# Kernel tuning notes

Hardware: AMD Instinct MI355X
Metric: run time of the kernel (lower is better)

Reference implementation:

```python
import math
import jax, jax.numpy as jnp
import numpy as np

LM_DAMPING = 1e-3
MOTION_LAMBDA = 1.0
LM_ITERS = (2, 3, 4)


def _skew(w):  # (B,3) -> (B,3,3)
    z = jnp.zeros_like(w[:, 0])
    return jnp.stack([z, -w[:, 2], w[:, 1],
                      w[:, 2], z, -w[:, 0],
                      -w[:, 1], w[:, 0], z], axis=-1).reshape(-1, 3, 3)


def _se3_exp(xi):  # (B,6) -> (B,4,4)
    t, w = xi[:, :3], xi[:, 3:]
    theta = jnp.clip(jnp.linalg.norm(w, axis=-1, keepdims=True), 1e-8, None)  # (B,1)
    K = _skew(w / theta)
    eye = jnp.eye(3, dtype=xi.dtype)
    st = jnp.sin(theta)[:, :, None]          # (B,1,1)
    ct = (1.0 - jnp.cos(theta))[:, :, None]
    KK = K @ K
    R = eye + st * K + ct * KK
    th = jnp.clip(theta[:, :, None], 1e-8, None)
    V = eye + (ct / th) * K + (1.0 - st / th) * KK
    t_out = (V @ t[..., None])[..., 0]
    B = xi.shape[0]
    T = jnp.tile(jnp.eye(4, dtype=xi.dtype)[None], (B, 1, 1))
    T = T.at[:, :3, :3].set(R).at[:, :3, 3].set(t_out)
    return T


def _se3_log(T):  # (B,4,4) -> (B,6)
    R, t = T[:, :3, :3], T[:, :3, 3]
    cos_a = (R[:, 0, 0] + R[:, 1, 1] + R[:, 2, 2] - 1.0) / 2.0
    theta = jnp.arccos(jnp.clip(cos_a, -1.0 + 1e-7, 1.0 - 1e-7))
    small = jnp.abs(theta) < 1e-6
    th = jnp.clip(theta, 1e-8, None)
    w = jnp.stack([R[:, 2, 1] - R[:, 1, 2],
                   R[:, 0, 2] - R[:, 2, 0],
                   R[:, 1, 0] - R[:, 0, 1]], axis=-1)
    w = w / (2.0 * jnp.clip(jnp.sin(th), 1e-8, None))[:, None] * th[:, None]
    w = jnp.where(small[:, None], 0.0, w)
    return jnp.concatenate([t, w], axis=-1)


def _sample_one(feat, gx, gy):
    # feat (C,H,W); gx,gy (P,) normalized in [-1,1]; align_corners=False, border padding
    C, H, W = feat.shape
    x = jnp.clip(((gx + 1.0) * W - 1.0) / 2.0, 0.0, W - 1)
    y = jnp.clip(((gy + 1.0) * H - 1.0) / 2.0, 0.0, H - 1)
    x0 = jnp.floor(x); y0 = jnp.floor(y)
    x1 = jnp.minimum(x0 + 1.0, W - 1); y1 = jnp.minimum(y0 + 1.0, H - 1)
    wx = x - x0; wy = y - y0
    x0i, x1i = x0.astype(jnp.int32), x1.astype(jnp.int32)
    y0i, y1i = y0.astype(jnp.int32), y1.astype(jnp.int32)
    f00 = feat[:, y0i, x0i]; f01 = feat[:, y0i, x1i]
    f10 = feat[:, y1i, x0i]; f11 = feat[:, y1i, x1i]
    return (f00 * (1 - wx) * (1 - wy) + f01 * wx * (1 - wy)
            + f10 * (1 - wx) * wy + f11 * wx * wy)  # (C,P)

_sample = jax.vmap(_sample_one, in_axes=(0, 0, 0))


def _generate_hypotheses(T_pred, key):
    rng = jnp.arange(-11.0, 13.0, 2.0, dtype=jnp.float32)  # 12 values
    pg, yg = jnp.meshgrid(rng, rng, indexing='ij')
    pitch = pg.reshape(-1) * (math.pi / 180.0)
    yaw = yg.reshape(-1) * (math.pi / 180.0)
    M = pitch.shape[0]  # 144
    t_noise = jax.random.normal(key, (M, 3), dtype=jnp.float32) * 1.0  # translation_std
    xi = jnp.stack([t_noise[:, 0], t_noise[:, 1], t_noise[:, 2],
                    jnp.zeros(M, jnp.float32), pitch, yaw], axis=-1)
    dT = _se3_exp(xi)  # (M,4,4)
    return jnp.einsum('mij,bjk->bmik', dT, T_pred)  # (B,M,4,4)


def _residuals(T, q_feat, r_feat, q_unc, geo, K, level):
    # T (B,M,4,4); fallback path evaluates only first min(M,16) hypotheses
    B, M = T.shape[:2]
    _, C, H, W = q_feat.shape
    scale = 1.0 / (4.0 / 2 ** level)
    Ks = jnp.concatenate([K[:, :2] * scale, K[:, 2:]], axis=1)
    M16 = min(M, 16)
    Tm = T[:, :M16]  # (B,16,4,4)
    N = geo.shape[1]
    pts_h = jnp.concatenate([geo, jnp.ones((B, N, 1), geo.dtype)], axis=-1)  # (B,N,4)
    pts_cam = jnp.einsum('bmij,bnj->bmni', Tm[:, :, :3, :], pts_h)  # (B,16,N,3)
    z = jnp.clip(pts_cam[..., 2:3], 1e-6, None)
    xy = pts_cam[..., :2] / z
    fx = Ks[:, 0, 0][:, None, None]; fy = Ks[:, 1, 1][:, None, None]
    cx = Ks[:, 0, 2][:, None, None]; cy = Ks[:, 1, 2][:, None, None]
    u = fx * xy[..., 0] + cx
    v = fy * xy[..., 1] + cy
    gx = (2.0 * u / max(W - 1, 1) - 1.0).reshape(B, M16 * N)
    gy = (2.0 * v / max(H - 1, 1) - 1.0).reshape(B, M16 * N)
    qs = _sample(q_feat, gx, gy).reshape(B, C, M16, N)
    rs = _sample(r_feat, gx, gy).reshape(B, C, M16, N)
    diff2 = (qs - rs) ** 2
    unc = _sample(q_unc, gx, gy).reshape(B, 1, M16, N)
    res = (diff2 * unc).sum(axis=1).mean(axis=-1)  # (B,16)
    return jnp.zeros((B, M), T.dtype).at[:, :M16].set(res)


def reference(T_pred, geo_anchors, intrinsics, q0, q1, q2, r0, r1, r2, u0, u1, u2):
    key = jax.random.key(42)
    B = T_pred.shape[0]
    T_cur = _generate_hypotheses(T_pred, jax.random.fold_in(key, 0))
    M = T_cur.shape[1]
    q_feats = (q0, q1, q2); r_feats = (r0, r1, r2); uncs = (u0, u1, u2)
    costs = jnp.zeros((B, M), T_pred.dtype)
    for level, n_iters in enumerate(LM_ITERS):
        for it in range(n_iters):
            res = _residuals(T_cur, q_feats[level], r_feats[level], uncs[level],
                             geo_anchors, intrinsics, level)
            damping = LM_DAMPING * 0.5 ** level
            noise = jax.random.normal(jax.random.fold_in(key, 100 + level * 10 + it),
                                      (B, M, 6), dtype=T_pred.dtype)
            step = -damping * res[..., None] * noise * 0.01
            delta = _se3_exp(step.reshape(B * M, 6)).reshape(B, M, 4, 4)
            T_cur = delta @ T_cur
            costs = res
    # motion-constrained selection: C_total = C_photo + lambda * ||log(T_ref T_pred^-1)||
    T_rel = T_cur @ jnp.linalg.inv(T_pred)[:, None]
    geod = jnp.linalg.norm(_se3_log(T_rel.reshape(B * M, 4, 4)), axis=-1).reshape(B, M)
    total = costs + MOTION_LAMBDA * geod
    idx = jnp.argmin(total, axis=1)
    T_best = jnp.take_along_axis(T_cur, idx[:, None, None, None], axis=1)[:, 0]
    return T_best, costs


def setup_inputs() -> dict:
    key = jax.random.key(0)
    ks = jax.random.split(key, 16)
    B, N = 8, 500
    # valid SE(3) predicted poses (small perturbation of identity)
    T_pred = _se3_exp(jax.random.normal(ks[0], (B, 6), jnp.float32) * 0.1)
    # 3D anchors in front of the camera (z ~ 6)
    geo = jax.random.uniform(ks[1], (B, N, 3), jnp.float32, -2.0, 2.0)
    geo = geo.at[..., 2].add(6.0)
    K = jnp.tile(jnp.array([[200.0, 0.0, 128.0],
                            [0.0, 200.0, 96.0],
                            [0.0, 0.0, 1.0]], jnp.float32)[None], (B, 1, 1))
    shapes_f = [(B, 128, 48, 64), (B, 64, 96, 128), (B, 32, 192, 256)]
    q = [jax.random.normal(ks[2 + i], s, jnp.float32) for i, s in enumerate(shapes_f)]
    r = [jax.random.normal(ks[5 + i], s, jnp.float32) for i, s in enumerate(shapes_f)]
    u = [jax.random.uniform(ks[8 + i], (s[0], 1, s[2], s[3]), jnp.float32)
         for i, s in enumerate(shapes_f)]
    return {"T_pred": T_pred, "geo_anchors": geo, "intrinsics": K,
            "q0": q[0], "q1": q[1], "q2": q[2],
            "r0": r[0], "r1": r[1], "r2": r[2],
            "u0": u[0], "u1": u[1], "u2": u[2]}
```

## Files before the change

### kernel.cpp

```cpp
#include <hip/hip_runtime.h>
#include <stdint.h>
#include <math.h>

#define JAX_PARTITIONABLE 1

#define NB 8
#define NM 144
#define NM16 16
#define NPTS 500
#define GP 16

__host__ __device__ __forceinline__ uint32_t rotl32(uint32_t x, int r) {
    return (x << r) | (x >> (32 - r));
}

__host__ __device__ inline void threefry2x32(uint32_t k0, uint32_t k1,
                                             uint32_t x0, uint32_t x1,
                                             uint32_t& o0, uint32_t& o1) {
    uint32_t ks2 = k0 ^ k1 ^ 0x1BD11BDAu;
    x0 += k0; x1 += k1;
    const int RA[4] = {13, 15, 26, 6};
    const int RB[4] = {17, 29, 16, 24};
#define R4(ROT) { x0 += x1; x1 = rotl32(x1, ROT[0]); x1 ^= x0; \
                  x0 += x1; x1 = rotl32(x1, ROT[1]); x1 ^= x0; \
                  x0 += x1; x1 = rotl32(x1, ROT[2]); x1 ^= x0; \
                  x0 += x1; x1 = rotl32(x1, ROT[3]); x1 ^= x0; }
    R4(RA); x0 += k1;  x1 += ks2 + 1u;
    R4(RB); x0 += ks2; x1 += k0 + 2u;
    R4(RA); x0 += k0;  x1 += k1 + 3u;
    R4(RB); x0 += k1;  x1 += ks2 + 4u;
    R4(RA); x0 += ks2; x1 += k0 + 5u;
#undef R4
    o0 = x0; o1 = x1;
}

__device__ __forceinline__ float erfinv32(float x) {
    float w = -log1pf(-x * x);
    float p;
    if (w < 5.0f) {
        w = w - 2.5f;
        p = 2.81022636e-08f;
        p = fmaf(p, w, 3.43273939e-07f);
        p = fmaf(p, w, -3.5233877e-06f);
        p = fmaf(p, w, -4.39150654e-06f);
        p = fmaf(p, w, 0.00021858087f);
        p = fmaf(p, w, -0.00125372503f);
        p = fmaf(p, w, -0.00417768164f);
        p = fmaf(p, w, 0.246640727f);
        p = fmaf(p, w, 1.50140941f);
    } else {
        w = sqrtf(w) - 3.0f;
        p = -0.000200214257f;
        p = fmaf(p, w, 0.000100950558f);
        p = fmaf(p, w, 0.00134934322f);
        p = fmaf(p, w, -0.00367342844f);
        p = fmaf(p, w, 0.00573950773f);
        p = fmaf(p, w, -0.0076224613f);
        p = fmaf(p, w, 0.00943887047f);
        p = fmaf(p, w, 1.00167406f);
        p = fmaf(p, w, 2.83297682f);
    }
    return p * x;
}

__device__ __forceinline__ float jax_normal(uint32_t k0, uint32_t k1,
                                            uint32_t idx, uint32_t half) {
    uint32_t o0, o1, bits;
#if JAX_PARTITIONABLE
    threefry2x32(k0, k1, 0u, idx, o0, o1);
    bits = o0 ^ o1;
#else
    if (idx < half) { threefry2x32(k0, k1, idx, idx + half, o0, o1); bits = o0; }
    else            { threefry2x32(k0, k1, idx - half, idx, o0, o1); bits = o1; }
#endif
    uint32_t fb = (bits >> 9) | 0x3F800000u;
    float f = __uint_as_float(fb) - 1.0f;
    const float lo = -0.99999994f;
    float u = f * (1.0f - lo) + lo;
    u = fmaxf(lo, u);
    return 1.4142135623730951f * erfinv32(u);
}

__device__ inline void se3_exp6(const float xi[6], float T[12]) {
    float tx = xi[0], ty = xi[1], tz = xi[2];
    float wx = xi[3], wy = xi[4], wz = xi[5];
    float nrm = sqrtf(wx * wx + wy * wy + wz * wz);
    float theta = fmaxf(nrm, 1e-8f);
    float kx = wx / theta, ky = wy / theta, kz = wz / theta;
    float K[9] = {0.0f, -kz, ky, kz, 0.0f, -kx, -ky, kx, 0.0f};
    float st = sinf(theta);
    float ct = 1.0f - cosf(theta);
    float KK[9];
    for (int i = 0; i < 3; i++)
        for (int j = 0; j < 3; j++)
            KK[i * 3 + j] = K[i * 3 + 0] * K[0 + j] + K[i * 3 + 1] * K[3 + j] + K[i * 3 + 2] * K[6 + j];
    float a = ct / theta;
    float bb = 1.0f - st / theta;
    float R[9], V[9];
    for (int i = 0; i < 3; i++)
        for (int j = 0; j < 3; j++) {
            float e = (i == j) ? 1.0f : 0.0f;
            R[i * 3 + j] = e + st * K[i * 3 + j] + ct * KK[i * 3 + j];
            V[i * 3 + j] = e + a * K[i * 3 + j] + bb * KK[i * 3 + j];
        }
    float t0 = V[0] * tx + V[1] * ty + V[2] * tz;
    float t1 = V[3] * tx + V[4] * ty + V[5] * tz;
    float t2 = V[6] * tx + V[7] * ty + V[8] * tz;
    T[0] = R[0]; T[1] = R[1]; T[2] = R[2];  T[3] = t0;
    T[4] = R[3]; T[5] = R[4]; T[6] = R[5];  T[7] = t1;
    T[8] = R[6]; T[9] = R[7]; T[10] = R[8]; T[11] = t2;
}

__device__ inline void compose44(const float dT[12], const float P[16], float Tn[16]) {
    for (int i = 0; i < 3; i++)
        for (int j = 0; j < 4; j++)
            Tn[i * 4 + j] = dT[i * 4 + 0] * P[0 + j] + dT[i * 4 + 1] * P[4 + j] +
                            dT[i * 4 + 2] * P[8 + j] + dT[i * 4 + 3] * P[12 + j];
    Tn[12] = 0.0f; Tn[13] = 0.0f; Tn[14] = 0.0f; Tn[15] = 1.0f;
}

__device__ inline void make_hypothesis(int m, const float* P, uint32_t hk0, uint32_t hk1,
                                       float Tn[16]) {
    float tn[3];
    for (int c = 0; c < 3; c++)
        tn[c] = jax_normal(hk0, hk1, (uint32_t)(m * 3 + c), 216u);
    int gi = m / 12, gj = m % 12;
    const float d2r = (float)(M_PI / 180.0);
    float xi[6] = {tn[0], tn[1], tn[2], 0.0f,
                   (float)(2 * gi - 11) * d2r, (float)(2 * gj - 11) * d2r};
    float dT[12];
    se3_exp6(xi, dT);
    compose44(dT, P, Tn);
}

__device__ inline void se3_exp6d(const double xi[6], double T[12]) {
    double tx = xi[0], ty = xi[1], tz = xi[2];
    double wx = xi[3], wy = xi[4], wz = xi[5];
    double nrm = sqrt(wx * wx + wy * wy + wz * wz);
    double theta = fmax(nrm, 1e-8);
    double kx = wx / theta, ky = wy / theta, kz = wz / theta;
    double K[9] = {0.0, -kz, ky, kz, 0.0, -kx, -ky, kx, 0.0};
    double st = sin(theta);
    double ct = 1.0 - cos(theta);
    double KK[9];
    for (int i = 0; i < 3; i++)
        for (int j = 0; j < 3; j++)
            KK[i * 3 + j] = K[i * 3 + 0] * K[0 + j] + K[i * 3 + 1] * K[3 + j] + K[i * 3 + 2] * K[6 + j];
    double a = ct / theta;
    double bb = 1.0 - st / theta;
    double R[9], V[9];
    for (int i = 0; i < 3; i++)
        for (int j = 0; j < 3; j++) {
            double e = (i == j) ? 1.0 : 0.0;
            R[i * 3 + j] = e + st * K[i * 3 + j] + ct * KK[i * 3 + j];
            V[i * 3 + j] = e + a * K[i * 3 + j] + bb * KK[i * 3 + j];
        }
    double t0 = V[0] * tx + V[1] * ty + V[2] * tz;
    double t1 = V[3] * tx + V[4] * ty + V[5] * tz;
    double t2 = V[6] * tx + V[7] * ty + V[8] * tz;
    T[0] = R[0]; T[1] = R[1]; T[2] = R[2];  T[3] = t0;
    T[4] = R[3]; T[5] = R[4]; T[6] = R[5];  T[7] = t1;
    T[8] = R[6]; T[9] = R[7]; T[10] = R[8]; T[11] = t2;
}

__device__ inline void compose44d(const double dT[12], const double P[16], double Tn[16]) {
    for (int i = 0; i < 3; i++)
        for (int j = 0; j < 4; j++)
            Tn[i * 4 + j] = dT[i * 4 + 0] * P[0 + j] + dT[i * 4 + 1] * P[4 + j] +
                            dT[i * 4 + 2] * P[8 + j] + dT[i * 4 + 3] * P[12 + j];
    Tn[12] = 0.0; Tn[13] = 0.0; Tn[14] = 0.0; Tn[15] = 1.0;
}

__device__ inline void make_hypothesis_d(int m, const double* P, uint32_t hk0, uint32_t hk1,
                                         double Tn[16]) {
    float tn[3];
    for (int c = 0; c < 3; c++)
        tn[c] = jax_normal(hk0, hk1, (uint32_t)(m * 3 + c), 216u);
    int gi = m / 12, gj = m % 12;
    const float d2r = (float)(M_PI / 180.0);
    float pf = (float)(2 * gi - 11) * d2r;
    float yf = (float)(2 * gj - 11) * d2r;
    double xi[6] = {(double)tn[0], (double)tn[1], (double)tn[2], 0.0,
                    (double)pf, (double)yf};
    double dT[12];
    se3_exp6d(xi, dT);
    compose44d(dT, P, Tn);
}

struct IterKeys { uint32_t k0[9]; uint32_t k1[9]; float damping[9]; };

template <int C, int H, int W, int PX, int GRP>
__device__ void gram_body(const float* __restrict__ q, const float* __restrict__ r,
                          const float* __restrict__ u, float* __restrict__ G,
                          float* part, int blk) {
    constexpr int HW = H * W;
    constexpr int TPB = HW / PX;
    constexpr int CPG = C / GRP;
    const int b = blk / TPB;
    const int tile = blk % TPB;
    const int tid = threadIdx.x;
    const int g = tid / PX;
    const int p = tid % PX;
    const int px = tile * PX + p;
    const int y = px / W, x = px % W;
    const int x1 = (x + 1 < W) ? x + 1 : W - 1;
    const int y1 = (y + 1 < H) ? y + 1 : H - 1;
    const int i00 = y * W + x,  i01 = y * W + x1;
    const int i10 = y1 * W + x, i11 = y1 * W + x1;

    const size_t cb = ((size_t)b * C + g * CPG) * HW;
    const float* qp = q + cb;
    const float* rp = r + cb;
    float acc[10];
#pragma unroll
    for (int i = 0; i < 10; i++) acc[i] = 0.0f;
#pragma unroll 4
    for (int c = 0; c < CPG; c++) {
        float d00 = qp[i00] - rp[i00];
        float d01 = qp[i01] - rp[i01];
        float d10 = qp[i10] - rp[i10];
        float d11 = qp[i11] - rp[i11];
        acc[0] = fmaf(d00, d00, acc[0]);
        acc[1] = fmaf(d00, d01, acc[1]);
        acc[2] = fmaf(d00, d10, acc[2]);
        acc[3] = fmaf(d00, d11, acc[3]);
        acc[4] = fmaf(d01, d01, acc[4]);
        acc[5] = fmaf(d01, d10, acc[5]);
        acc[6] = fmaf(d01, d11, acc[6]);
        acc[7] = fmaf(d10, d10, acc[7]);
        acc[8] = fmaf(d10, d11, acc[8]);
        acc[9] = fmaf(d11, d11, acc[9]);
        qp += HW; rp += HW;
    }
    if (GRP > 1) {
#pragma unroll
        for (int i = 0; i < 10; i++) part[(g * 10 + i) * PX + p] = acc[i];
        __syncthreads();
        if (tid < PX) {
#pragma unroll
            for (int i = 0; i < 10; i++) {
                float s = part[i * PX + p];
                for (int gg = 1; gg < GRP; gg++) s += part[(gg * 10 + i) * PX + p];
                acc[i] = s;
            }
        }
    }
    if (tid < PX) {
        const size_t ub = (size_t)b * HW;
        float u00 = u[ub + i00], u01 = u[ub + i01];
        float u10 = u[ub + i10], u11 = u[ub + i11];
        size_t base = ((size_t)b * HW + px) * GP;
        float4 g0 = {acc[0], acc[1], acc[2], acc[3]};
        float4 g1 = {acc[4], acc[5], acc[6], acc[7]};
        float4 g2 = {acc[8], acc[9], u00, u01};
        float4 g3 = {u10, u11, 0.0f, 0.0f};
        *(float4*)(G + base + 0)  = g0;
        *(float4*)(G + base + 4)  = g1;
        *(float4*)(G + base + 8)  = g2;
        *(float4*)(G + base + 12) = g3;
    }
}

#define NBLK0 384
#define NBLK1 768
#define NBLK2 1536

__global__ __launch_bounds__(256) void gram_fused_kernel(
    const float* __restrict__ q0, const float* __restrict__ r0, const float* __restrict__ u0,
    float* __restrict__ G0,
    const float* __restrict__ q1, const float* __restrict__ r1, const float* __restrict__ u1,
    float* __restrict__ G1,
    const float* __restrict__ q2, const float* __restrict__ r2, const float* __restrict__ u2,
    float* __restrict__ G2) {
    __shared__ float part[2560];
    const int blk = blockIdx.x;
    if (blk < NBLK0)
        gram_body<128, 48, 64, 64, 4>(q0, r0, u0, G0, part, blk);
    else if (blk < NBLK0 + NBLK1)
        gram_body<64, 96, 128, 128, 2>(q1, r1, u1, G1, part, blk - NBLK0);
    else
        gram_body<32, 192, 256, 256, 1>(q2, r2, u2, G2, part, blk - NBLK0 - NBLK1);
}

template <int H, int W>
__device__ void run_level_gram(const float* __restrict__ Gb,
                               float fx, float fy, float cx, float cy,
                               const float* geoS, float* Tsh, float* red, float* resS,
                               float* stepS, float* out, int b, int m,
                               const IterKeys& iks, int firstIter, int niter) {
    const int tid = threadIdx.x;
    for (int it = 0; it < niter; it++) {
        const int iter = firstIter + it;
        float acc = 0.0f;
        if (tid < NPTS) {
            float px = geoS[tid * 3], py = geoS[tid * 3 + 1], pz = geoS[tid * 3 + 2];
            float X = Tsh[0] * px + Tsh[1] * py + Tsh[2]  * pz + Tsh[3];
            float Y = Tsh[4] * px + Tsh[5] * py + Tsh[6]  * pz + Tsh[7];
            float Z = Tsh[8] * px + Tsh[9] * py + Tsh[10] * pz + Tsh[11];
            float z = fmaxf(Z, 1e-6f);
            float uu = fx * (X / z) + cx;
            float vv = fy * (Y / z) + cy;
            float gx = 2.0f * uu / (float)(W - 1) - 1.0f;
            float gy = 2.0f * vv / (float)(H - 1) - 1.0f;
            float x = fminf(fmaxf(((gx + 1.0f) * (float)W - 1.0f) * 0.5f, 0.0f), (float)(W - 1));
            float y = fminf(fmaxf(((gy + 1.0f) * (float)H - 1.0f) * 0.5f, 0.0f), (float)(H - 1));
            float x0f = floorf(x), y0f = floorf(y);
            float wx = x - x0f, wy = y - y0f;
            int x0i = (int)x0f, y0i = (int)y0f;
            int i00 = y0i * W + x0i;
            float w00 = (1.0f - wx) * (1.0f - wy), w01 = wx * (1.0f - wy);
            float w10 = (1.0f - wx) * wy,          w11 = wx * wy;
            const float* Gp = Gb + (size_t)i00 * GP;
            float4 g0 = *(const float4*)(Gp + 0);
            float4 g1 = *(const float4*)(Gp + 4);
            float4 g2 = *(const float4*)(Gp + 8);
            float4 g3 = *(const float4*)(Gp + 12);
            float uval = w00 * g2.z + w01 * g2.w + w10 * g3.x + w11 * g3.y;
            float val = w00 * w00 * g0.x + w01 * w01 * g1.x +
                        w10 * w10 * g1.w + w11 * w11 * g2.y +
                        2.0f * (w00 * w01 * g0.y + w00 * w10 * g0.z + w00 * w11 * g0.w +
                                w01 * w10 * g1.y + w01 * w11 * g1.z + w10 * w11 * g2.x);
            acc = uval * val;
        }
        float v = acc;
        for (int off = 32; off > 0; off >>= 1) v += __shfl_down(v, off, 64);
        if ((tid & 63) == 0) red[tid >> 6] = v;
        __syncthreads();
        if (tid == 0) {
            float s = 0.0f;
            for (int w = 0; w < 8; w++) s += red[w];
            float res = s / 500.0f;
            *resS = res;
            if (iter == 8) out[128 + b * NM + m] = res;
        }
        __syncthreads();
        if (tid < 6) {
            uint32_t fi = (uint32_t)((b * NM + m) * 6 + tid);
            float nz = jax_normal(iks.k0[iter], iks.k1[iter], fi, 3456u);
            stepS[tid] = (((-iks.damping[iter]) * (*resS)) * nz) * 0.01f;
        }
        __syncthreads();
        if (tid == 0) {
            float xi[6];
            for (int j = 0; j < 6; j++) xi[j] = stepS[j];
            float dT[12];
            se3_exp6(xi, dT);
            float Told[16];
            for (int k = 0; k < 16; k++) Told[k] = Tsh[k];
            float Tn[16];
            compose44(dT, Told, Tn);
            for (int k = 0; k < 16; k++) Tsh[k] = Tn[k];
        }
        __syncthreads();
    }
}

__global__ __launch_bounds__(512) void evolve_kernel_gram(
    const float* __restrict__ T_pred, const float* __restrict__ geo,
    const float* __restrict__ Kmat,
    const float* __restrict__ G0, const float* __restrict__ G1, const float* __restrict__ G2,
    float* __restrict__ Tws, float* __restrict__ out,
    uint32_t hk0, uint32_t hk1, IterKeys iks) {
    const int bm = blockIdx.x;
    const int b = bm & 7;
    const int m = bm >> 3;
    const int tid = threadIdx.x;

    __shared__ float Tsh[16];
    __shared__ float geoS[NPTS * 3];
    __shared__ float red[8];
    __shared__ float resS;
    __shared__ float stepS[6];

    for (int i = tid; i < NPTS * 3; i += 512) geoS[i] = geo[b * NPTS * 3 + i];

    if (tid == 0) {
        float P[16];
        for (int k = 0; k < 16; k++) P[k] = T_pred[b * 16 + k];
        float Tn[16];
        make_hypothesis(m, P, hk0, hk1, Tn);
        for (int k = 0; k < 16; k++) Tsh[k] = Tn[k];
    }
    __syncthreads();

    float K00 = Kmat[b * 9 + 0], K02 = Kmat[b * 9 + 2];
    float K11 = Kmat[b * 9 + 4], K12 = Kmat[b * 9 + 5];

    run_level_gram<48, 64>(G0 + (size_t)b * 48 * 64 * GP,
                           K00 * 0.25f, K11 * 0.25f, K02 * 0.25f, K12 * 0.25f,
                           geoS, Tsh, red, &resS, stepS, out, b, m, iks, 0, 2);
    run_level_gram<96, 128>(G1 + (size_t)b * 96 * 128 * GP,
                            K00 * 0.5f, K11 * 0.5f, K02 * 0.5f, K12 * 0.5f,
                            geoS, Tsh, red, &resS, stepS, out, b, m, iks, 2, 3);
    run_level_gram<192, 256>(G2 + (size_t)b * 192 * 256 * GP,
                             K00, K11, K02, K12,
                             geoS, Tsh, red, &resS, stepS, out, b, m, iks, 5, 4);

    if (tid < 16) Tws[(size_t)(b * NM16 + m) * 16 + tid] = Tsh[tid];
}

template <int C, int H, int W>
__device__ void run_level_nchw(const float* __restrict__ qb, const float* __restrict__ rb,
                               const float* __restrict__ ub,
                               float fx, float fy, float cx, float cy,
                               const float* geoS, float* Tsh, float* red, float* resS,
                               float* stepS, float* out, int b, int m,
                               const IterKeys& iks, int firstIter, int niter) {
    const int tid = threadIdx.x;
    const int HW = H * W;
    for (int it = 0; it < niter; it++) {
        const int iter = firstIter + it;
        float acc = 0.0f;
        if (tid < NPTS) {
            float px = geoS[tid * 3], py = geoS[tid * 3 + 1], pz = geoS[tid * 3 + 2];
            float X = Tsh[0] * px + Tsh[1] * py + Tsh[2]  * pz + Tsh[3];
            float Y = Tsh[4] * px + Tsh[5] * py + Tsh[6]  * pz + Tsh[7];
            float Z = Tsh[8] * px + Tsh[9] * py + Tsh[10] * pz + Tsh[11];
            float z = fmaxf(Z, 1e-6f);
            float uu = fx * (X / z) + cx;
            float vv = fy * (Y / z) + cy;
            float gx = 2.0f * uu / (float)(W - 1) - 1.0f;
            float gy = 2.0f * vv / (float)(H - 1) - 1.0f;
            float x = fminf(fmaxf(((gx + 1.0f) * (float)W - 1.0f) * 0.5f, 0.0f), (float)(W - 1));
            float y = fminf(fmaxf(((gy + 1.0f) * (float)H - 1.0f) * 0.5f, 0.0f), (float)(H - 1));
            float x0f = floorf(x), y0f = floorf(y);
            float x1f = fminf(x0f + 1.0f, (float)(W - 1));
            float y1f = fminf(y0f + 1.0f, (float)(H - 1));
            float wx = x - x0f, wy = y - y0f;
            int x0i = (int)x0f, x1i = (int)x1f, y0i = (int)y0f, y1i = (int)y1f;
            int i00 = y0i * W + x0i, i01 = y0i * W + x1i;
            int i10 = y1i * W + x0i, i11 = y1i * W + x1i;
            float w00 = (1.0f - wx) * (1.0f - wy), w01 = wx * (1.0f - wy);
            float w10 = (1.0f - wx) * wy,          w11 = wx * wy;
            float uval = ub[i00] * w00 + ub[i01] * w01 + ub[i10] * w10 + ub[i11] * w11;
            const float* qp = qb;
            const float* rp = rb;
#pragma unroll 4
            for (int c = 0; c < C; c++) {
                float qv = qp[i00] * w00 + qp[i01] * w01 + qp[i10] * w10 + qp[i11] * w11;
                float rv = rp[i00] * w00 + rp[i01] * w01 + rp[i10] * w10 + rp[i11] * w11;
                float d = qv - rv;
                acc += uval * (d * d);
                qp += HW; rp += HW;
            }
        }
        float v = acc;
        for (int off = 32; off > 0; off >>= 1) v += __shfl_down(v, off, 64);
        if ((tid & 63) == 0) red[tid >> 6] = v;
        __syncthreads();
        if (tid == 0) {
            float s = 0.0f;
            for (int w = 0; w < 8; w++) s += red[w];
            float res = s / 500.0f;
            *resS = res;
            if (iter == 8) out[128 + b * NM + m] = res;
        }
        __syncthreads();
        if (tid < 6) {
            uint32_t fi = (uint32_t)((b * NM + m) * 6 + tid);
            float nz = jax_normal(iks.k0[iter], iks.k1[iter], fi, 3456u);
            stepS[tid] = (((-iks.damping[iter]) * (*resS)) * nz) * 0.01f;
        }
        __syncthreads();
        if (tid == 0) {
            float xi[6];
            for (int j = 0; j < 6; j++) xi[j] = stepS[j];
            float dT[12];
            se3_exp6(xi, dT);
            float Told[16];
            for (int k = 0; k < 16; k++) Told[k] = Tsh[k];
            float Tn[16];
            compose44(dT, Told, Tn);
            for (int k = 0; k < 16; k++) Tsh[k] = Tn[k];
        }
        __syncthreads();
    }
}

__global__ __launch_bounds__(512) void evolve_kernel_nchw(
    const float* __restrict__ T_pred, const float* __restrict__ geo,
    const float* __restrict__ Kmat,
    const float* __restrict__ q0, const float* __restrict__ q1, const float* __restrict__ q2,
    const float* __restrict__ r0, const float* __restrict__ r1, const float* __restrict__ r2,
    const float* __restrict__ u0, const float* __restrict__ u1, const float* __restrict__ u2,
    float* __restrict__ Tws, float* __restrict__ out,
    uint32_t hk0, uint32_t hk1, IterKeys iks) {
    const int bm = blockIdx.x;
    const int b = bm >> 4;
    const int m = bm & 15;
    const int tid = threadIdx.x;

    __shared__ float Tsh[16];
    __shared__ float geoS[NPTS * 3];
    __shared__ float red[8];
    __shared__ float resS;
    __shared__ float stepS[6];

    for (int i = tid; i < NPTS * 3; i += 512) geoS[i] = geo[b * NPTS * 3 + i];

    if (tid == 0) {
        float P[16];
        for (int k = 0; k < 16; k++) P[k] = T_pred[b * 16 + k];
        float Tn[16];
        make_hypothesis(m, P, hk0, hk1, Tn);
        for (int k = 0; k < 16; k++) Tsh[k] = Tn[k];
    }
    __syncthreads();

    float K00 = Kmat[b * 9 + 0], K02 = Kmat[b * 9 + 2];
    float K11 = Kmat[b * 9 + 4], K12 = Kmat[b * 9 + 5];

    run_level_nchw<128, 48, 64>(q0 + (size_t)b * 128 * 48 * 64, r0 + (size_t)b * 128 * 48 * 64,
                                u0 + (size_t)b * 48 * 64,
                                K00 * 0.25f, K11 * 0.25f, K02 * 0.25f, K12 * 0.25f,
                                geoS, Tsh, red, &resS, stepS, out, b, m, iks, 0, 2);
    run_level_nchw<64, 96, 128>(q1 + (size_t)b * 64 * 96 * 128, r1 + (size_t)b * 64 * 96 * 128,
                                u1 + (size_t)b * 96 * 128,
                                K00 * 0.5f, K11 * 0.5f, K02 * 0.5f, K12 * 0.5f,
                                geoS, Tsh, red, &resS, stepS, out, b, m, iks, 2, 3);
    run_level_nchw<32, 192, 256>(q2 + (size_t)b * 32 * 192 * 256, r2 + (size_t)b * 32 * 192 * 256,
                                 u2 + (size_t)b * 192 * 256,
                                 K00, K11, K02, K12,
                                 geoS, Tsh, red, &resS, stepS, out, b, m, iks, 5, 4);

    if (tid < 16) Tws[(size_t)bm * 16 + tid] = Tsh[tid];
}

__global__ __launch_bounds__(192) void finalize_kernel(
    const float* __restrict__ T_pred, const float* __restrict__ Tws,
    float* __restrict__ out, uint32_t hk0, uint32_t hk1) {
    const int b = blockIdx.x;
    const int tid = threadIdx.x;
    __shared__ double Pm[16];
    __shared__ double inv[12];
    __shared__ double totals[NM];
    __shared__ int bestm_sh;

    if (tid < 16) Pm[tid] = (double)T_pred[b * 16 + tid];
    __syncthreads();
    if (tid == 0) {
        for (int k = 0; k < 3; k++)
            for (int j = 0; j < 3; j++) inv[k * 4 + j] = Pm[j * 4 + k];
        for (int k = 0; k < 3; k++)
            inv[k * 4 + 3] = -(Pm[0 * 4 + k] * Pm[3] + Pm[1 * 4 + k] * Pm[7] + Pm[2 * 4 + k] * Pm[11]);
    }
    __syncthreads();

    double Tc[16];
    if (tid < NM) {
        double cost;
        if (tid < NM16) {
            for (int k = 0; k < 16; k++) Tc[k] = (double)Tws[(size_t)(b * NM16 + tid) * 16 + k];
            cost = (double)out[128 + b * NM + tid];
        } else {
            make_hypothesis_d(tid, Pm, hk0, hk1, Tc);
            cost = 0.0;
            out[128 + b * NM + tid] = 0.0f;
        }
        double Tr[12];
        for (int i = 0; i < 3; i++)
            for (int j = 0; j < 4; j++)
                Tr[i * 4 + j] = Tc[i * 4 + 0] * inv[0 + j] + Tc[i * 4 + 1] * inv[4 + j] +
                                Tc[i * 4 + 2] * inv[8 + j] + ((j == 3) ? Tc[i * 4 + 3] : 0.0);
        double cos_a = (Tr[0] + Tr[5] + Tr[10] - 1.0) * 0.5;
        cos_a = fmin(fmax(cos_a, -1.0 + 1e-7), 1.0 - 1e-7);
        double theta = acos(cos_a);
        double th = fmax(theta, 1e-8);
        double s2 = 2.0 * fmax(sin(th), 1e-8);
        double w0 = (Tr[2 * 4 + 1] - Tr[1 * 4 + 2]) / s2 * th;
        double w1 = (Tr[0 * 4 + 2] - Tr[2 * 4 + 0]) / s2 * th;
        double w2 = (Tr[1 * 4 + 0] - Tr[0 * 4 + 1]) / s2 * th;
        double t0 = Tr[3], t1 = Tr[7], t2 = Tr[11];
        double geod = sqrt(t0 * t0 + t1 * t1 + t2 * t2 + w0 * w0 + w1 * w1 + w2 * w2);
        totals[tid] = cost + geod;
    }
    __syncthreads();
    if (tid == 0) {
        int best = 0;
        double bv = totals[0];
        for (int mm = 1; mm < NM; mm++) {
            if (totals[mm] < bv) { bv = totals[mm]; best = mm; }
        }
        bestm_sh = best;
    }
    __syncthreads();
    if (tid == bestm_sh) {
        for (int k = 0; k < 16; k++) out[b * 16 + k] = (float)Tc[k];
    }
}

extern "C" void kernel_launch(void* const* d_in, const int* in_sizes, int n_in,
                              void* d_out, int out_size, void* d_ws, size_t ws_size,
                              hipStream_t stream) {
    (void)in_sizes; (void)n_in; (void)out_size;
    const float* T_pred = (const float*)d_in[0];
    const float* geo    = (const float*)d_in[1];
    const float* K      = (const float*)d_in[2];
    const float* q0 = (const float*)d_in[3];
    const float* q1 = (const float*)d_in[4];
    const float* q2 = (const float*)d_in[5];
    const float* r0 = (const float*)d_in[6];
    const float* r1 = (const float*)d_in[7];
    const float* r2 = (const float*)d_in[8];
    const float* u0 = (const float*)d_in[9];
    const float* u1 = (const float*)d_in[10];
    const float* u2 = (const float*)d_in[11];
    float* out = (float*)d_out;

    float* Tws = (float*)d_ws;
    const size_t nG0 = (size_t)NB * 48 * 64 * GP;
    const size_t nG1 = (size_t)NB * 96 * 128 * GP;
    const size_t nG2 = (size_t)NB * 192 * 256 * GP;
    float* G0 = Tws + 2048;
    float* G1 = G0 + nG0;
    float* G2 = G1 + nG1;
    const size_t need = (2048 + nG0 + nG1 + nG2) * sizeof(float);

    uint32_t hk0, hk1;
    threefry2x32(0u, 42u, 0u, 0u, hk0, hk1);
    IterKeys iks;
    const int seeds[9] = {100, 101, 110, 111, 112, 120, 121, 122, 123};
    const float damp[9] = {0.001f, 0.001f, 0.0005f, 0.0005f, 0.0005f,
                           0.00025f, 0.00025f, 0.00025f, 0.00025f};
    for (int i = 0; i < 9; i++) {
        threefry2x32(0u, 42u, 0u, (uint32_t)seeds[i], iks.k0[i], iks.k1[i]);
        iks.damping[i] = damp[i];
    }

    if (ws_size >= need) {
        gram_fused_kernel<<<dim3(NBLK0 + NBLK1 + NBLK2), dim3(256), 0, stream>>>(
            q0, r0, u0, G0, q1, r1, u1, G1, q2, r2, u2, G2);
        evolve_kernel_gram<<<dim3(NB * NM16), dim3(512), 0, stream>>>(
            T_pred, geo, K, G0, G1, G2, Tws, out, hk0, hk1, iks);
    } else {
        evolve_kernel_nchw<<<dim3(NB * NM16), dim3(512), 0, stream>>>(
            T_pred, geo, K, q0, q1, q2, r0, r1, r2, u0, u1, u2, Tws, out, hk0, hk1, iks);
    }
    finalize_kernel<<<dim3(NB), dim3(192), 0, stream>>>(T_pred, Tws, out, hk0, hk1);
}
```

Before: 274.3 us.

## Vectorize gram precompute: four pixels per thread with float4 loads and lane shuffles

Each thread in the gram precompute now handles four adjacent pixels. It loads q, r and u rows with float4 and gets the right-neighbour value from the next lane via __shfl_down instead of issuing separate scalar loads for the x+1 neighbour. This cuts redundant global loads and the block count by four, but uses 40 accumulators per thread and more shared memory for the cross-group reduction, which may lower occupancy. Correctness at wave boundaries relies on four-pixel groups never crossing a row end except at the edge flag, which holds because each row width is a multiple of 4 times 64.

```diff
diff --git a/kernel.cpp b/kernel.cpp
--- a/kernel.cpp
+++ b/kernel.cpp
@@ -189,81 +189,117 @@
 
 struct IterKeys { uint32_t k0[9]; uint32_t k1[9]; float damping[9]; };
 
-template <int C, int H, int W, int PX, int GRP>
-__device__ void gram_body(const float* __restrict__ q, const float* __restrict__ r,
-                          const float* __restrict__ u, float* __restrict__ G,
-                          float* part, int blk) {
+template <int C, int H, int W, int GRP>
+__device__ void gram_body_v(const float* __restrict__ q, const float* __restrict__ r,
+                            const float* __restrict__ u, float* __restrict__ G,
+                            float* part, int blk) {
     constexpr int HW = H * W;
-    constexpr int TPB = HW / PX;
+    constexpr int PT = 256 / GRP;
+    constexpr int PPB = PT * 4;
+    constexpr int TPB = HW / PPB;
     constexpr int CPG = C / GRP;
     const int b = blk / TPB;
     const int tile = blk % TPB;
     const int tid = threadIdx.x;
-    const int g = tid / PX;
-    const int p = tid % PX;
-    const int px = tile * PX + p;
-    const int y = px / W, x = px % W;
-    const int x1 = (x + 1 < W) ? x + 1 : W - 1;
+    const int g = tid / PT;
+    const int p = tid % PT;
+    const int px0 = tile * PPB + p * 4;
+    const int y = px0 / W;
+    const int x0 = px0 - y * W;
     const int y1 = (y + 1 < H) ? y + 1 : H - 1;
-    const int i00 = y * W + x,  i01 = y * W + x1;
-    const int i10 = y1 * W + x, i11 = y1 * W + x1;
-
-    const size_t cb = ((size_t)b * C + g * CPG) * HW;
-    const float* qp = q + cb;
-    const float* rp = r + cb;
-    float acc[10];
-#pragma unroll
-    for (int i = 0; i < 10; i++) acc[i] = 0.0f;
-#pragma unroll 4
+    const bool edge = (x0 + 4 >= W);
+
+    const int rb0 = y * W + x0;
+    const int rb1 = y1 * W + x0;
+    const float* qp = q + ((size_t)b * C + (size_t)g * CPG) * HW;
+    const float* rp = r + ((size_t)b * C + (size_t)g * CPG) * HW;
+
+    float acc[4][10];
+#pragma unroll
+    for (int j = 0; j < 4; j++)
+#pragma unroll
+        for (int i = 0; i < 10; i++) acc[j][i] = 0.0f;
+
+#pragma unroll 2
     for (int c = 0; c < CPG; c++) {
-        float d00 = qp[i00] - rp[i00];
-        float d01 = qp[i01] - rp[i01];
-        float d10 = qp[i10] - rp[i10];
-        float d11 = qp[i11] - rp[i11];
-        acc[0] = fmaf(d00, d00, acc[0]);
-        acc[1] = fmaf(d00, d01, acc[1]);
-        acc[2] = fmaf(d00, d10, acc[2]);
-        acc[3] = fmaf(d00, d11, acc[3]);
-        acc[4] = fmaf(d01, d01, acc[4]);
-        acc[5] = fmaf(d01, d10, acc[5]);
-        acc[6] = fmaf(d01, d11, acc[6]);
-        acc[7] = fmaf(d10, d10, acc[7]);
-        acc[8] = fmaf(d10, d11, acc[8]);
-        acc[9] = fmaf(d11, d11, acc[9]);
+        float4 a0 = *(const float4*)(qp + rb0);
+        float4 a1 = *(const float4*)(qp + rb1);
+        float4 b0 = *(const float4*)(rp + rb0);
+        float4 b1 = *(const float4*)(rp + rb1);
         qp += HW; rp += HW;
+        float e0[5], e1[5];
+        e0[0] = a0.x - b0.x; e0[1] = a0.y - b0.y; e0[2] = a0.z - b0.z; e0[3] = a0.w - b0.w;
+        e1[0] = a1.x - b1.x; e1[1] = a1.y - b1.y; e1[2] = a1.z - b1.z; e1[3] = a1.w - b1.w;
+        float d0n = __shfl_down(e0[0], 1, 64);
+        float d1n = __shfl_down(e1[0], 1, 64);
+        e0[4] = edge ? e0[3] : d0n;
+        e1[4] = edge ? e1[3] : d1n;
+#pragma unroll
+        for (int j = 0; j < 4; j++) {
+            float d00 = e0[j], d01 = e0[j + 1];
+            float d10 = e1[j], d11 = e1[j + 1];
+            acc[j][0] = fmaf(d00, d00, acc[j][0]);
+            acc[j][1] = fmaf(d00, d01, acc[j][1]);
+            acc[j][2] = fmaf(d00, d10, acc[j][2]);
+            acc[j][3] = fmaf(d00, d11, acc[j][3]);
+            acc[j][4] = fmaf(d01, d01, acc[j][4]);
+            acc[j][5] = fmaf(d01, d10, acc[j][5]);
+            acc[j][6] = fmaf(d01, d11, acc[j][6]);
+            acc[j][7] = fmaf(d10, d10, acc[j][7]);
+            acc[j][8] = fmaf(d10, d11, acc[j][8]);
+            acc[j][9] = fmaf(d11, d11, acc[j][9]);
+        }
     }
     if (GRP > 1) {
-#pragma unroll
-        for (int i = 0; i < 10; i++) part[(g * 10 + i) * PX + p] = acc[i];
-        __syncthreads();
-        if (tid < PX) {
-#pragma unroll
-            for (int i = 0; i < 10; i++) {
-                float s = part[i * PX + p];
-                for (int gg = 1; gg < GRP; gg++) s += part[(gg * 10 + i) * PX + p];
-                acc[i] = s;
+        if (g > 0) {
+            float* pp = part + (size_t)(g - 1) * 40 * PT;
+#pragma unroll
+            for (int j = 0; j < 4; j++)
+#pragma unroll
+                for (int i = 0; i < 10; i++)
+                    pp[(j * 10 + i) * PT + p] = acc[j][i];
+        }
+        __syncthreads();
+        if (g == 0) {
+            for (int gg = 1; gg < GRP; gg++) {
+                const float* pp = part + (size_t)(gg - 1) * 40 * PT;
+#pragma unroll
+                for (int j = 0; j < 4; j++)
+#pragma unroll
+                    for (int i = 0; i < 10; i++)
+                        acc[j][i] += pp[(j * 10 + i) * PT + p];
             }
         }
     }
-    if (tid < PX) {
-        const size_t ub = (size_t)b * HW;
-        float u00 = u[ub + i00], u01 = u[ub + i01];
-        float u10 = u[ub + i10], u11 = u[ub + i11];
-        size_t base = ((size_t)b * HW + px) * GP;
-        float4 g0 = {acc[0], acc[1], acc[2], acc[3]};
-        float4 g1 = {acc[4], acc[5], acc[6], acc[7]};
-        float4 g2 = {acc[8], acc[9], u00, u01};
-        float4 g3 = {u10, u11, 0.0f, 0.0f};
-        *(float4*)(G + base + 0)  = g0;
-        *(float4*)(G + base + 4)  = g1;
-        *(float4*)(G + base + 8)  = g2;
-        *(float4*)(G + base + 12) = g3;
-    }
-}
-
-#define NBLK0 384
-#define NBLK1 768
-#define NBLK2 1536
+    if (g == 0) {
+        const float* ub = u + (size_t)b * HW;
+        float4 u0 = *(const float4*)(ub + rb0);
+        float4 u1 = *(const float4*)(ub + rb1);
+        float w0[5], w1[5];
+        w0[0] = u0.x; w0[1] = u0.y; w0[2] = u0.z; w0[3] = u0.w;
+        w1[0] = u1.x; w1[1] = u1.y; w1[2] = u1.z; w1[3] = u1.w;
+        float u0n = __shfl_down(u0.x, 1, 64);
+        float u1n = __shfl_down(u1.x, 1, 64);
+        w0[4] = edge ? w0[3] : u0n;
+        w1[4] = edge ? w1[3] : u1n;
+#pragma unroll
+        for (int j = 0; j < 4; j++) {
+            size_t base = ((size_t)b * HW + px0 + j) * GP;
+            float4 g0v = {acc[j][0], acc[j][1], acc[j][2], acc[j][3]};
+            float4 g1v = {acc[j][4], acc[j][5], acc[j][6], acc[j][7]};
+            float4 g2v = {acc[j][8], acc[j][9], w0[j], w0[j + 1]};
+            float4 g3v = {w1[j], w1[j + 1], 0.0f, 0.0f};
+            *(float4*)(G + base + 0)  = g0v;
+            *(float4*)(G + base + 4)  = g1v;
+            *(float4*)(G + base + 8)  = g2v;
+            *(float4*)(G + base + 12) = g3v;
+        }
+    }
+}
+
+#define VBLK0 96
+#define VBLK1 192
+#define VBLK2 384
 
 __global__ __launch_bounds__(256) void gram_fused_kernel(
     const float* __restrict__ q0, const float* __restrict__ r0, const float* __restrict__ u0,
@@ -272,14 +308,14 @@
     float* __restrict__ G1,
     const float* __restrict__ q2, const float* __restrict__ r2, const float* __restrict__ u2,
     float* __restrict__ G2) {
-    __shared__ float part[2560];
+    __shared__ float part[3 * 40 * 64];
     const int blk = blockIdx.x;
-    if (blk < NBLK0)
-        gram_body<128, 48, 64, 64, 4>(q0, r0, u0, G0, part, blk);
-    else if (blk < NBLK0 + NBLK1)
-        gram_body<64, 96, 128, 128, 2>(q1, r1, u1, G1, part, blk - NBLK0);
+    if (blk < VBLK0)
+        gram_body_v<128, 48, 64, 4>(q0, r0, u0, G0, part, blk);
+    else if (blk < VBLK0 + VBLK1)
+        gram_body_v<64, 96, 128, 2>(q1, r1, u1, G1, part, blk - VBLK0);
     else
-        gram_body<32, 192, 256, 256, 1>(q2, r2, u2, G2, part, blk - NBLK0 - NBLK1);
+        gram_body_v<32, 192, 256, 1>(q2, r2, u2, G2, part, blk - VBLK0 - VBLK1);
 }
 
 template <int H, int W>
@@ -628,7 +664,7 @@
     }
 
     if (ws_size >= need) {
-        gram_fused_kernel<<<dim3(NBLK0 + NBLK1 + NBLK2), dim3(256), 0, stream>>>(
+        gram_fused_kernel<<<dim3(VBLK0 + VBLK1 + VBLK2), dim3(256), 0, stream>>>(
             q0, r0, u0, G0, q1, r1, u1, G1, q2, r2, u2, G2);
         evolve_kernel_gram<<<dim3(NB * NM16), dim3(512), 0, stream>>>(
             T_pred, geo, K, G0, G1, G2, Tws, out, hk0, hk1, iks);
```

New measurement: 256.9 us. 1.07x faster.
